# Optimization experiments

Hardware: AMD Instinct MI355X
Metric: run time of the kernel (lower is better)

Reference implementation:

```python
import jax, jax.numpy as jnp
import numpy as np

N, E = 50000, 400000
FN, FE = 128, 128          # in/out node and edge feature dims
W = 256                     # fnns_width
EPS = 1e-5


def _layer_norm(x, g, b):
    m = x.mean(-1, keepdims=True)
    var = x.var(-1, keepdims=True)
    return (x - m) / jnp.sqrt(var + EPS) * g + b


def _fnn(x, params):
    # FNN applies ReLU after EVERY linear, including the last one.
    for w, b in params:
        x = jax.nn.relu(x @ w + b)
    return x


def setup_inputs() -> dict:
    key = jax.random.key(0)
    ks = jax.random.split(key, 32)
    s = 0.05
    d = {
        'v': jax.random.normal(ks[0], (N, FN), jnp.float32),
        'e': jax.random.normal(ks[1], (E, FE), jnp.float32),
        'edge_index': jax.random.randint(ks[2], (2, E), 0, N, jnp.int32),
        # edge branch: LayerNorm over concat width FE + 2*FN = 384
        'edge_ln_g': jnp.ones((FE + 2 * FN,), jnp.float32),
        'edge_ln_b': jnp.zeros((FE + 2 * FN,), jnp.float32),
        'ew0': jax.random.normal(ks[3], (FE + 2 * FN, W), jnp.float32) * s,
        'eb0': jnp.zeros((W,), jnp.float32),
        'ew1': jax.random.normal(ks[4], (W, W), jnp.float32) * s,
        'eb1': jnp.zeros((W,), jnp.float32),
        'ew2': jax.random.normal(ks[5], (W, FE), jnp.float32) * s,
        'eb2': jnp.zeros((FE,), jnp.float32),
        'edge_linear': jax.random.normal(ks[6], (FE, FE), jnp.float32) * s,
        # node branch: LayerNorm over concat width FE + FN = 256
        'node_ln_g': jnp.ones((FE + FN,), jnp.float32),
        'node_ln_b': jnp.zeros((FE + FN,), jnp.float32),
        'nw0': jax.random.normal(ks[7], (FE + FN, W), jnp.float32) * s,
        'nb0': jnp.zeros((W,), jnp.float32),
        'nw1': jax.random.normal(ks[8], (W, W), jnp.float32) * s,
        'nb1': jnp.zeros((W,), jnp.float32),
        'nw2': jax.random.normal(ks[9], (W, FN), jnp.float32) * s,
        'nb2': jnp.zeros((FN,), jnp.float32),
        'node_linear': jax.random.normal(ks[10], (FN, FN), jnp.float32) * s,
    }
    return d


def reference(v, e, edge_index, edge_ln_g, edge_ln_b, ew0, eb0, ew1, eb1,
              ew2, eb2, edge_linear, node_ln_g, node_ln_b, nw0, nb0, nw1,
              nb1, nw2, nb2, node_linear):
    row, col = edge_index[0], edge_index[1]
    n = v.shape[0]
    # edge update: residual linear + FNN(LayerNorm(concat))
    edge_in = jnp.concatenate([e, v[row], v[col]], axis=-1)  # [E, 384]
    e_new = e @ edge_linear + _fnn(
        _layer_norm(edge_in, edge_ln_g, edge_ln_b),
        [(ew0, eb0), (ew1, eb1), (ew2, eb2)])
    # mean scatter-aggregate over destination nodes (col)
    counts = jax.ops.segment_sum(jnp.ones((e.shape[0],), e.dtype), col,
                                 num_segments=n)
    e_aggr = jax.ops.segment_sum(e_new, col, num_segments=n)
    e_aggr = e_aggr / jnp.clip(counts, 1.0)[:, None]
    # node update
    node_in = jnp.concatenate([e_aggr, v], axis=-1)  # [N, 256]
    v_new = v @ node_linear + _fnn(
        _layer_norm(node_in, node_ln_g, node_ln_b),
        [(nw0, nb0), (nw1, nb1), (nw2, nb2)])
    return (v_new, e_new)
```

## Files before the change

### kernel.cpp

```cpp
#include <hip/hip_runtime.h>

typedef _Float16 f16_t;
typedef f16_t f16x4 __attribute__((ext_vector_type(4)));
typedef f16_t f16x8 __attribute__((ext_vector_type(8)));
typedef float f32x4 __attribute__((ext_vector_type(4)));

#define MFMA16(a, b, c) __builtin_amdgcn_mfma_f32_16x16x32_f16((a), (b), (c), 0, 0, 0)

__device__ __forceinline__ float bfr(float x) { return (float)(__bf16)x; }

__global__ void pack_weights_kernel(
    const float* __restrict__ ew0, const float* __restrict__ ew1,
    const float* __restrict__ ew2, const float* __restrict__ eL,
    const float* __restrict__ nw0, const float* __restrict__ nw1,
    const float* __restrict__ nw2, const float* __restrict__ nL,
    f16_t* __restrict__ dst)
{
    int tid = blockIdx.x * 256 + threadIdx.x;
    int fid = tid >> 6, lane = tid & 63;
    const float* src; int Ncols, foff, doff;
    if (fid < 192)      { src = ew0; Ncols = 256; foff = 0;   doff = 0;      }
    else if (fid < 320) { src = ew1; Ncols = 256; foff = 192; doff = 98304;  }
    else if (fid < 384) { src = ew2; Ncols = 128; foff = 320; doff = 163840; }
    else if (fid < 416) { src = eL;  Ncols = 128; foff = 384; doff = 196608; }
    else if (fid < 544) { src = nw0; Ncols = 256; foff = 416; doff = 212992; }
    else if (fid < 672) { src = nw1; Ncols = 256; foff = 544; doff = 278528; }
    else if (fid < 736) { src = nw2; Ncols = 128; foff = 672; doff = 344064; }
    else                { src = nL;  Ncols = 128; foff = 736; doff = 376832; }
    int f = fid - foff;
    int NT = Ncols >> 4;
    int kstep = f / NT, ntile = f - kstep * NT;
    int col = ntile * 16 + (lane & 15);
    int kbase = kstep * 32 + ((lane >> 4) << 3);
    f16x8 out;
    #pragma unroll
    for (int j = 0; j < 8; ++j)
        out[j] = (f16_t)bfr(src[(size_t)(kbase + j) * Ncols + col]);
    *reinterpret_cast<f16x8*>(dst + (size_t)doff + ((size_t)f * 64 + lane) * 8) = out;
}

__launch_bounds__(1024, 8)
__global__ void edge_kernel(
    const float* __restrict__ vfeat, const float* __restrict__ efeat,
    const int* __restrict__ eidx,
    const float* __restrict__ lng, const float* __restrict__ lnb,
    const f16_t* __restrict__ pw,
    const float* __restrict__ b0, const float* __restrict__ b1,
    const float* __restrict__ b2,
    float* __restrict__ out_e, float* __restrict__ aggr, float* __restrict__ cnts,
    int Ee)
{
    __shared__ f16_t XF[24576];
    __shared__ f16_t ERF[8192];
    __shared__ int cidx[64];

    const int t    = threadIdx.x;
    const int lane = t & 63;
    const int wv   = t >> 6;
    const int cw   = wv & 7;
    const int rw   = wv >> 3;
    const size_t ebase = (size_t)blockIdx.x * 64;

    const int el = t >> 4;
    const int pp = t & 15;
    const int et0 = el >> 4;
    const size_t eg0 = ebase + el;
    const int r0 = eidx[eg0];
    const int c0 = eidx[(size_t)Ee + eg0];

    float s = 0.f, sq = 0.f;
    {
        const float4* e4 = (const float4*)efeat;
        const float4* v4 = (const float4*)vfeat;
        #pragma unroll
        for (int i = 0; i < 6; ++i) {
            int q = i * 16 + pp;
            float4 r;
            if (q < 32)      r = e4[eg0 * 32 + q];
            else if (q < 64) r = v4[(size_t)r0 * 32 + (q - 32)];
            else             r = v4[(size_t)c0 * 32 + (q - 64)];
            r.x = bfr(r.x); r.y = bfr(r.y); r.z = bfr(r.z); r.w = bfr(r.w);
            f16x4 h;
            h[0] = (f16_t)r.x; h[1] = (f16_t)r.y; h[2] = (f16_t)r.z; h[3] = (f16_t)r.w;
            int lanep = (el & 15) + 16 * ((q & 7) >> 1);
            int idx = ((q >> 3) * 4 + et0) * 512 + lanep * 8 + (q & 1) * 4;
            *reinterpret_cast<f16x4*>(&XF[idx]) = h;
            if (q < 32)
                *reinterpret_cast<f16x4*>(&ERF[idx]) = h;
            s  += r.x + r.y + r.z + r.w;
            sq += r.x*r.x + r.y*r.y + r.z*r.z + r.w*r.w;
        }
        if (pp == 0) {
            cidx[el] = c0;
            unsafeAtomicAdd(&cnts[c0], 1.0f);
        }
    }
    #pragma unroll
    for (int off = 1; off < 16; off <<= 1) {
        s  += __shfl_xor(s, off);
        sq += __shfl_xor(sq, off);
    }
    const float mean = s * (1.f / 384.f);
    const float rstd = 1.f / sqrtf(sq * (1.f / 384.f) - mean * mean + 1e-5f);

    {
        const float4* g4p = (const float4*)lng;
        const float4* bpp = (const float4*)lnb;
        #pragma unroll
        for (int i = 0; i < 6; ++i) {
            int q = i * 16 + pp;
            int lanep = (el & 15) + 16 * ((q & 7) >> 1);
            int idx = ((q >> 3) * 4 + et0) * 512 + lanep * 8 + (q & 1) * 4;
            f16x4 h = *reinterpret_cast<f16x4*>(&XF[idx]);
            float4 g = g4p[q]; float4 bb = bpp[q];
            h[0] = (f16_t)(((float)h[0] - mean) * rstd * bfr(g.x) + bfr(bb.x));
            h[1] = (f16_t)(((float)h[1] - mean) * rstd * bfr(g.y) + bfr(bb.y));
            h[2] = (f16_t)(((float)h[2] - mean) * rstd * bfr(g.z) + bfr(bb.z));
            h[3] = (f16_t)(((float)h[3] - mean) * rstd * bfr(g.w) + bfr(bb.w));
            *reinterpret_cast<f16x4*>(&XF[idx]) = h;
        }
    }
    __syncthreads();

    const int r16 = lane & 15;
    const int g4i = lane >> 4;

    {
        f32x4 acc[2][2] = {};
        const f16_t* bw = pw;
        #pragma unroll
        for (int ks = 0; ks < 12; ++ks) {
            f16x8 wa0 = *reinterpret_cast<const f16x8*>(
                &bw[((size_t)(ks * 16 + cw * 2 + 0) * 64 + lane) * 8]);
            f16x8 wa1 = *reinterpret_cast<const f16x8*>(
                &bw[((size_t)(ks * 16 + cw * 2 + 1) * 64 + lane) * 8]);
            #pragma unroll
            for (int e2 = 0; e2 < 2; ++e2) {
                f16x8 xb = *reinterpret_cast<const f16x8*>(
                    &XF[(ks * 4 + rw * 2 + e2) * 512 + lane * 8]);
                acc[e2][0] = MFMA16(wa0, xb, acc[e2][0]);
                acc[e2][1] = MFMA16(wa1, xb, acc[e2][1]);
            }
        }
        __syncthreads();
        #pragma unroll
        for (int F2 = 0; F2 < 2; ++F2) {
            int cbase = (cw * 2 + F2) * 16 + g4i * 4;
            float4 bs = *reinterpret_cast<const float4*>(&b0[cbase]);
            float bias[4] = { bfr(bs.x), bfr(bs.y), bfr(bs.z), bfr(bs.w) };
            int lane2 = r16 + 16 * ((cbase & 31) >> 3);
            int j0 = cbase & 7;
            #pragma unroll
            for (int e2 = 0; e2 < 2; ++e2) {
                f16x4 hv;
                #pragma unroll
                for (int qi = 0; qi < 4; ++qi)
                    hv[qi] = (f16_t)fmaxf(acc[e2][F2][qi] + bias[qi], 0.f);
                int idx = ((cbase >> 5) * 4 + rw * 2 + e2) * 512 + lane2 * 8 + j0;
                *reinterpret_cast<f16x4*>(&XF[idx]) = hv;
            }
        }
    }
    __syncthreads();

    {
        f32x4 acc[2][2] = {};
        const f16_t* bw = pw + 98304;
        #pragma unroll
        for (int ks = 0; ks < 8; ++ks) {
            f16x8 wa0 = *reinterpret_cast<const f16x8*>(
                &bw[((size_t)(ks * 16 + cw * 2 + 0) * 64 + lane) * 8]);
            f16x8 wa1 = *reinterpret_cast<const f16x8*>(
                &bw[((size_t)(ks * 16 + cw * 2 + 1) * 64 + lane) * 8]);
            #pragma unroll
            for (int e2 = 0; e2 < 2; ++e2) {
                f16x8 xb = *reinterpret_cast<const f16x8*>(
                    &XF[(ks * 4 + rw * 2 + e2) * 512 + lane * 8]);
                acc[e2][0] = MFMA16(wa0, xb, acc[e2][0]);
                acc[e2][1] = MFMA16(wa1, xb, acc[e2][1]);
            }
        }
        __syncthreads();
        #pragma unroll
        for (int F2 = 0; F2 < 2; ++F2) {
            int cbase = (cw * 2 + F2) * 16 + g4i * 4;
            float4 bs = *reinterpret_cast<const float4*>(&b1[cbase]);
            float bias[4] = { bfr(bs.x), bfr(bs.y), bfr(bs.z), bfr(bs.w) };
            int lane2 = r16 + 16 * ((cbase & 31) >> 3);
            int j0 = cbase & 7;
            #pragma unroll
            for (int e2 = 0; e2 < 2; ++e2) {
                f16x4 hv;
                #pragma unroll
                for (int qi = 0; qi < 4; ++qi)
                    hv[qi] = (f16_t)fmaxf(acc[e2][F2][qi] + bias[qi], 0.f);
                int idx = ((cbase >> 5) * 4 + rw * 2 + e2) * 512 + lane2 * 8 + j0;
                *reinterpret_cast<f16x4*>(&XF[idx]) = hv;
            }
        }
    }
    __syncthreads();

    {
        f32x4 accF[2] = {}, accR[2] = {};
        const f16_t* bw = pw + 163840;
        #pragma unroll
        for (int ks = 0; ks < 8; ++ks) {
            f16x8 wb = *reinterpret_cast<const f16x8*>(
                &bw[((size_t)(ks * 8 + cw) * 64 + lane) * 8]);
            #pragma unroll
            for (int e2 = 0; e2 < 2; ++e2) {
                f16x8 xa = *reinterpret_cast<const f16x8*>(
                    &XF[(ks * 4 + rw * 2 + e2) * 512 + lane * 8]);
                accF[e2] = MFMA16(xa, wb, accF[e2]);
            }
        }
        const f16_t* bwL = pw + 196608;
        #pragma unroll
        for (int ks = 0; ks < 4; ++ks) {
            f16x8 wb = *reinterpret_cast<const f16x8*>(
                &bwL[((size_t)(ks * 8 + cw) * 64 + lane) * 8]);
            #pragma unroll
            for (int e2 = 0; e2 < 2; ++e2) {
                f16x8 ea = *reinterpret_cast<const f16x8*>(
                    &ERF[(ks * 4 + rw * 2 + e2) * 512 + lane * 8]);
                accR[e2] = MFMA16(ea, wb, accR[e2]);
            }
        }
        int c = cw * 16 + r16;
        float bias = bfr(b2[c]);
        #pragma unroll
        for (int e2 = 0; e2 < 2; ++e2)
            #pragma unroll
            for (int qi = 0; qi < 4; ++qi) {
                int rr = (rw * 2 + e2) * 16 + g4i * 4 + qi;
                float val = accR[e2][qi] + fmaxf(accF[e2][qi] + bias, 0.f);
                size_t eg2 = ebase + rr;
                out_e[eg2 * 128 + c] = val;
                unsafeAtomicAdd(&aggr[(size_t)cidx[rr] * 128 + c], val);
            }
    }
}

__launch_bounds__(512, 6)
__global__ void node_kernel(
    const float* __restrict__ vfeat, const float* __restrict__ aggr,
    const float* __restrict__ cnts,
    const float* __restrict__ lng, const float* __restrict__ lnb,
    const f16_t* __restrict__ pw,
    const float* __restrict__ b0, const float* __restrict__ b1,
    const float* __restrict__ b2,
    float* __restrict__ out_v, int Nn)
{
    __shared__ f16_t X[32 * 264];
    __shared__ f16_t H1[32 * 264];

    const int t    = threadIdx.x;
    const int lane = t & 63;
    const int wv   = t >> 6;
    const size_t nbase = (size_t)blockIdx.x * 32;

    const int nl = t >> 4;
    const int pp = t & 15;
    const size_t ng = nbase + nl;
    const bool valid = ng < (size_t)Nn;

    float4 d[4];
    float s = 0.f, sq = 0.f;
    {
        float cmax = 1.f;
        if (valid) cmax = fmaxf(cnts[ng], 1.f);
        const float4* a4 = (const float4*)aggr;
        const float4* v4 = (const float4*)vfeat;
        #pragma unroll
        for (int i = 0; i < 4; ++i) {
            int q = i * 16 + pp;
            float4 r = make_float4(0.f, 0.f, 0.f, 0.f);
            if (valid) {
                if (q < 32) {
                    r = a4[ng * 32 + q];
                    r.x = r.x / cmax; r.y = r.y / cmax;
                    r.z = r.z / cmax; r.w = r.w / cmax;
                } else {
                    float4 rv = v4[ng * 32 + (q - 32)];
                    r.x = bfr(rv.x); r.y = bfr(rv.y); r.z = bfr(rv.z); r.w = bfr(rv.w);
                }
            }
            d[i] = r;
            s  += r.x + r.y + r.z + r.w;
            sq += r.x*r.x + r.y*r.y + r.z*r.z + r.w*r.w;
        }
    }
    #pragma unroll
    for (int off = 1; off < 16; off <<= 1) {
        s  += __shfl_xor(s, off);
        sq += __shfl_xor(sq, off);
    }
    const float mean = s * (1.f / 256.f);
    const float rstd = 1.f / sqrtf(sq * (1.f / 256.f) - mean * mean + 1e-5f);
    {
        const float4* g4p = (const float4*)lng;
        const float4* bpp = (const float4*)lnb;
        #pragma unroll
        for (int i = 0; i < 4; ++i) {
            int q = i * 16 + pp;
            float4 g = g4p[q]; float4 bb = bpp[q];
            f16x4 y;
            y[0] = (f16_t)((d[i].x - mean) * rstd * bfr(g.x) + bfr(bb.x));
            y[1] = (f16_t)((d[i].y - mean) * rstd * bfr(g.y) + bfr(bb.y));
            y[2] = (f16_t)((d[i].z - mean) * rstd * bfr(g.z) + bfr(bb.z));
            y[3] = (f16_t)((d[i].w - mean) * rstd * bfr(g.w) + bfr(bb.w));
            *reinterpret_cast<f16x4*>(&X[nl * 264 + q * 4]) = y;
        }
    }
    __syncthreads();

    const int r16 = lane & 15;
    const int g4i = lane >> 4;
    const int cb4 = g4i * 4;

    {
        f32x4 acc[2][2] = {};
        const f16_t* bw = pw;
        #pragma unroll
        for (int ks = 0; ks < 8; ++ks) {
            f16x8 wa0 = *reinterpret_cast<const f16x8*>(
                &bw[((size_t)(ks * 16 + wv * 2 + 0) * 64 + lane) * 8]);
            f16x8 wa1 = *reinterpret_cast<const f16x8*>(
                &bw[((size_t)(ks * 16 + wv * 2 + 1) * 64 + lane) * 8]);
            #pragma unroll
            for (int nt = 0; nt < 2; ++nt) {
                f16x8 xb = *reinterpret_cast<const f16x8*>(
                    &X[(nt * 16 + r16) * 264 + ks * 32 + g4i * 8]);
                acc[nt][0] = MFMA16(wa0, xb, acc[nt][0]);
                acc[nt][1] = MFMA16(wa1, xb, acc[nt][1]);
            }
        }
        #pragma unroll
        for (int j = 0; j < 2; ++j) {
            int cb = (wv * 2 + j) * 16 + cb4;
            float4 bs = *reinterpret_cast<const float4*>(&b0[cb]);
            float bias[4] = { bfr(bs.x), bfr(bs.y), bfr(bs.z), bfr(bs.w) };
            #pragma unroll
            for (int nt = 0; nt < 2; ++nt) {
                f16x4 hv;
                #pragma unroll
                for (int qi = 0; qi < 4; ++qi)
                    hv[qi] = (f16_t)fmaxf(acc[nt][j][qi] + bias[qi], 0.f);
                *reinterpret_cast<f16x4*>(&H1[(nt * 16 + r16) * 264 + cb]) = hv;
            }
        }
    }
    __syncthreads();

    {
        f32x4 acc[2][2] = {};
        const f16_t* bw = pw + 65536;
        #pragma unroll
        for (int ks = 0; ks < 8; ++ks) {
            f16x8 wa0 = *reinterpret_cast<const f16x8*>(
                &bw[((size_t)(ks * 16 + wv * 2 + 0) * 64 + lane) * 8]);
            f16x8 wa1 = *reinterpret_cast<const f16x8*>(
                &bw[((size_t)(ks * 16 + wv * 2 + 1) * 64 + lane) * 8]);
            #pragma unroll
            for (int nt = 0; nt < 2; ++nt) {
                f16x8 xb = *reinterpret_cast<const f16x8*>(
                    &H1[(nt * 16 + r16) * 264 + ks * 32 + g4i * 8]);
                acc[nt][0] = MFMA16(wa0, xb, acc[nt][0]);
                acc[nt][1] = MFMA16(wa1, xb, acc[nt][1]);
            }
        }
        __syncthreads();
        #pragma unroll
        for (int j = 0; j < 2; ++j) {
            int cb = (wv * 2 + j) * 16 + cb4;
            float4 bs = *reinterpret_cast<const float4*>(&b1[cb]);
            float bias[4] = { bfr(bs.x), bfr(bs.y), bfr(bs.z), bfr(bs.w) };
            #pragma unroll
            for (int nt = 0; nt < 2; ++nt) {
                f16x4 hv;
                #pragma unroll
                for (int qi = 0; qi < 4; ++qi)
                    hv[qi] = (f16_t)fmaxf(acc[nt][j][qi] + bias[qi], 0.f);
                *reinterpret_cast<f16x4*>(&X[(nt * 16 + r16) * 264 + cb]) = hv;
            }
        }
    }
    __syncthreads();

    {
        f32x4 accF[2] = {}, accR[2] = {};
        const f16_t* bw = pw + 131072;
        #pragma unroll
        for (int ks = 0; ks < 8; ++ks) {
            f16x8 wb = *reinterpret_cast<const f16x8*>(
                &bw[((size_t)(ks * 8 + wv) * 64 + lane) * 8]);
            #pragma unroll
            for (int nt = 0; nt < 2; ++nt) {
                f16x8 xa = *reinterpret_cast<const f16x8*>(
                    &X[(nt * 16 + r16) * 264 + ks * 32 + g4i * 8]);
                accF[nt] = MFMA16(xa, wb, accF[nt]);
            }
        }
        const f16_t* bwL = pw + 163840;
        #pragma unroll
        for (int ks = 0; ks < 4; ++ks) {
            f16x8 wb = *reinterpret_cast<const f16x8*>(
                &bwL[((size_t)(ks * 8 + wv) * 64 + lane) * 8]);
            #pragma unroll
            for (int nt = 0; nt < 2; ++nt) {
                size_t rv = nbase + (size_t)(nt * 16 + r16);
                if (rv >= (size_t)Nn) rv = (size_t)Nn - 1;
                const float4* src = (const float4*)&vfeat[rv * 128 + ks * 32 + g4i * 8];
                float4 f0 = src[0];
                float4 f1 = src[1];
                f16x8 va;
                va[0] = (f16_t)bfr(f0.x); va[1] = (f16_t)bfr(f0.y);
                va[2] = (f16_t)bfr(f0.z); va[3] = (f16_t)bfr(f0.w);
                va[4] = (f16_t)bfr(f1.x); va[5] = (f16_t)bfr(f1.y);
                va[6] = (f16_t)bfr(f1.z); va[7] = (f16_t)bfr(f1.w);
                accR[nt] = MFMA16(va, wb, accR[nt]);
            }
        }
        int c = wv * 16 + r16;
        float bias = bfr(b2[c]);
        #pragma unroll
        for (int nt = 0; nt < 2; ++nt)
            #pragma unroll
            for (int qi = 0; qi < 4; ++qi) {
                int rr = nt * 16 + cb4 + qi;
                size_t ng2 = nbase + rr;
                if (ng2 < (size_t)Nn) {
                    float val = accR[nt][qi] + fmaxf(accF[nt][qi] + bias, 0.f);
                    out_v[ng2 * 128 + c] = val;
                }
            }
    }
}

extern "C" void kernel_launch(void* const* d_in, const int* in_sizes, int n_in,
                              void* d_out, int out_size, void* d_ws, size_t ws_size,
                              hipStream_t stream)
{
    const float* v    = (const float*)d_in[0];
    const float* e    = (const float*)d_in[1];
    const int*   eidx = (const int*)d_in[2];
    const float* elng = (const float*)d_in[3];
    const float* elnb = (const float*)d_in[4];
    const float* ew0  = (const float*)d_in[5];
    const float* eb0  = (const float*)d_in[6];
    const float* ew1  = (const float*)d_in[7];
    const float* eb1  = (const float*)d_in[8];
    const float* ew2  = (const float*)d_in[9];
    const float* eb2  = (const float*)d_in[10];
    const float* eLin = (const float*)d_in[11];
    const float* nlng = (const float*)d_in[12];
    const float* nlnb = (const float*)d_in[13];
    const float* nw0  = (const float*)d_in[14];
    const float* nb0  = (const float*)d_in[15];
    const float* nw1  = (const float*)d_in[16];
    const float* nb1  = (const float*)d_in[17];
    const float* nw2  = (const float*)d_in[18];
    const float* nb2  = (const float*)d_in[19];
    const float* nLin = (const float*)d_in[20];

    const int Nn = in_sizes[0] / 128;
    const int Ee = in_sizes[1] / 128;

    float* out_v = (float*)d_out;
    float* out_e = out_v + (size_t)Nn * 128;

    float* aggr = (float*)d_ws;
    float* cnts = aggr + (size_t)Nn * 128;
    f16_t* packw = (f16_t*)((char*)d_ws + (size_t)Nn * 129 * 4);

    hipMemsetAsync(d_ws, 0, (size_t)Nn * 129 * 4, stream);

    pack_weights_kernel<<<192, 256, 0, stream>>>(ew0, ew1, ew2, eLin,
                                                 nw0, nw1, nw2, nLin, packw);

    edge_kernel<<<(Ee + 63) / 64, 1024, 0, stream>>>(v, e, eidx, elng, elnb, packw,
                                                     eb0, eb1, eb2, out_e, aggr, cnts, Ee);

    node_kernel<<<(Nn + 31) / 32, 512, 0, stream>>>(v, aggr, cnts, nlng, nlnb,
                                                    packw + 212992, nb0, nb1, nb2,
                                                    out_v, Nn);
}
```

Measured before the change: 483.3 us.

## Remap edge kernel waves: each wave owns one output tile across all edges

```diff
diff --git a/kernel.cpp b/kernel.cpp
--- a/kernel.cpp
+++ b/kernel.cpp
@@ -50,158 +50,157 @@
     float* __restrict__ out_e, float* __restrict__ aggr, float* __restrict__ cnts,
     int Ee)
 {
-    __shared__ f16_t XF[24576];
-    __shared__ f16_t ERF[8192];
+    __shared__ f16_t XF[12 * 4 * 512];
+    __shared__ f16_t ERF[4 * 4 * 512];
+    __shared__ float SB[64 * 8];
     __shared__ int cidx[64];
 
     const int t    = threadIdx.x;
     const int lane = t & 63;
     const int wv   = t >> 6;
-    const int cw   = wv & 7;
-    const int rw   = wv >> 3;
+    const int r16  = lane & 15;
+    const int g4i  = lane >> 4;
     const size_t ebase = (size_t)blockIdx.x * 64;
 
-    const int el = t >> 4;
-    const int pp = t & 15;
-    const int et0 = el >> 4;
-    const size_t eg0 = ebase + el;
+    const int et_  = wv >> 2;
+    const int sq4  = wv & 3;
+    const int edge = et_ * 16 + r16;
+    const int slot = sq4 * 4 + g4i;
+    const size_t eg0 = ebase + edge;
     const int r0 = eidx[eg0];
     const int c0 = eidx[(size_t)Ee + eg0];
 
+    f16x8 oct[3];
     float s = 0.f, sq = 0.f;
     {
         const float4* e4 = (const float4*)efeat;
         const float4* v4 = (const float4*)vfeat;
-        #pragma unroll
-        for (int i = 0; i < 6; ++i) {
-            int q = i * 16 + pp;
-            float4 r;
-            if (q < 32)      r = e4[eg0 * 32 + q];
-            else if (q < 64) r = v4[(size_t)r0 * 32 + (q - 32)];
-            else             r = v4[(size_t)c0 * 32 + (q - 64)];
-            r.x = bfr(r.x); r.y = bfr(r.y); r.z = bfr(r.z); r.w = bfr(r.w);
-            f16x4 h;
-            h[0] = (f16_t)r.x; h[1] = (f16_t)r.y; h[2] = (f16_t)r.z; h[3] = (f16_t)r.w;
-            int lanep = (el & 15) + 16 * ((q & 7) >> 1);
-            int idx = ((q >> 3) * 4 + et0) * 512 + lanep * 8 + (q & 1) * 4;
-            *reinterpret_cast<f16x4*>(&XF[idx]) = h;
-            if (q < 32)
-                *reinterpret_cast<f16x4*>(&ERF[idx]) = h;
-            s  += r.x + r.y + r.z + r.w;
-            sq += r.x*r.x + r.y*r.y + r.z*r.z + r.w*r.w;
-        }
-        if (pp == 0) {
-            cidx[el] = c0;
+        const float4* srcs[3];
+        srcs[0] = &e4[eg0 * 32 + slot * 2];
+        srcs[1] = &v4[(size_t)r0 * 32 + slot * 2];
+        srcs[2] = &v4[(size_t)c0 * 32 + slot * 2];
+        #pragma unroll
+        for (int i = 0; i < 3; ++i) {
+            float4 f0 = srcs[i][0];
+            float4 f1 = srcs[i][1];
+            float x0 = bfr(f0.x), x1 = bfr(f0.y), x2 = bfr(f0.z), x3 = bfr(f0.w);
+            float x4 = bfr(f1.x), x5 = bfr(f1.y), x6 = bfr(f1.z), x7 = bfr(f1.w);
+            s  += x0 + x1 + x2 + x3 + x4 + x5 + x6 + x7;
+            sq += x0*x0 + x1*x1 + x2*x2 + x3*x3 + x4*x4 + x5*x5 + x6*x6 + x7*x7;
+            f16x8 h;
+            h[0] = (f16_t)x0; h[1] = (f16_t)x1; h[2] = (f16_t)x2; h[3] = (f16_t)x3;
+            h[4] = (f16_t)x4; h[5] = (f16_t)x5; h[6] = (f16_t)x6; h[7] = (f16_t)x7;
+            oct[i] = h;
+        }
+        *reinterpret_cast<f16x8*>(&ERF[(sq4 * 4 + et_) * 512 + lane * 8]) = oct[0];
+        if (slot == 0) {
+            cidx[edge] = c0;
             unsafeAtomicAdd(&cnts[c0], 1.0f);
         }
     }
-    #pragma unroll
-    for (int off = 1; off < 16; off <<= 1) {
-        s  += __shfl_xor(s, off);
-        sq += __shfl_xor(sq, off);
-    }
-    const float mean = s * (1.f / 384.f);
-    const float rstd = 1.f / sqrtf(sq * (1.f / 384.f) - mean * mean + 1e-5f);
-
-    {
+    s  += __shfl_xor(s, 16);  s  += __shfl_xor(s, 32);
+    sq += __shfl_xor(sq, 16); sq += __shfl_xor(sq, 32);
+    if (g4i == 0)
+        *reinterpret_cast<float2*>(&SB[edge * 8 + sq4 * 2]) = make_float2(s, sq);
+    __syncthreads();
+
+    {
+        float4 p0 = *reinterpret_cast<const float4*>(&SB[edge * 8]);
+        float4 p1 = *reinterpret_cast<const float4*>(&SB[edge * 8 + 4]);
+        float S = p0.x + p0.z + p1.x + p1.z;
+        float Q = p0.y + p0.w + p1.y + p1.w;
+        const float mean = S * (1.f / 384.f);
+        const float rstd = 1.f / sqrtf(Q * (1.f / 384.f) - mean * mean + 1e-5f);
         const float4* g4p = (const float4*)lng;
         const float4* bpp = (const float4*)lnb;
         #pragma unroll
-        for (int i = 0; i < 6; ++i) {
-            int q = i * 16 + pp;
-            int lanep = (el & 15) + 16 * ((q & 7) >> 1);
-            int idx = ((q >> 3) * 4 + et0) * 512 + lanep * 8 + (q & 1) * 4;
-            f16x4 h = *reinterpret_cast<f16x4*>(&XF[idx]);
-            float4 g = g4p[q]; float4 bb = bpp[q];
-            h[0] = (f16_t)(((float)h[0] - mean) * rstd * bfr(g.x) + bfr(bb.x));
-            h[1] = (f16_t)(((float)h[1] - mean) * rstd * bfr(g.y) + bfr(bb.y));
-            h[2] = (f16_t)(((float)h[2] - mean) * rstd * bfr(g.z) + bfr(bb.z));
-            h[3] = (f16_t)(((float)h[3] - mean) * rstd * bfr(g.w) + bfr(bb.w));
-            *reinterpret_cast<f16x4*>(&XF[idx]) = h;
-        }
-    }
-    __syncthreads();
-
-    const int r16 = lane & 15;
-    const int g4i = lane >> 4;
-
-    {
-        f32x4 acc[2][2] = {};
+        for (int i = 0; i < 3; ++i) {
+            int q = (i * 16 + slot) * 2;
+            float4 g0 = g4p[q], g1 = g4p[q + 1];
+            float4 bb0 = bpp[q], bb1 = bpp[q + 1];
+            f16x8 h = oct[i];
+            f16x8 y;
+            y[0] = (f16_t)(((float)h[0] - mean) * rstd * bfr(g0.x) + bfr(bb0.x));
+            y[1] = (f16_t)(((float)h[1] - mean) * rstd * bfr(g0.y) + bfr(bb0.y));
+            y[2] = (f16_t)(((float)h[2] - mean) * rstd * bfr(g0.z) + bfr(bb0.z));
+            y[3] = (f16_t)(((float)h[3] - mean) * rstd * bfr(g0.w) + bfr(bb0.w));
+            y[4] = (f16_t)(((float)h[4] - mean) * rstd * bfr(g1.x) + bfr(bb1.x));
+            y[5] = (f16_t)(((float)h[5] - mean) * rstd * bfr(g1.y) + bfr(bb1.y));
+            y[6] = (f16_t)(((float)h[6] - mean) * rstd * bfr(g1.z) + bfr(bb1.z));
+            y[7] = (f16_t)(((float)h[7] - mean) * rstd * bfr(g1.w) + bfr(bb1.w));
+            int ks = i * 4 + sq4;
+            *reinterpret_cast<f16x8*>(&XF[(ks * 4 + et_) * 512 + lane * 8]) = y;
+        }
+    }
+    __syncthreads();
+
+    {
+        f32x4 acc[4] = {};
         const f16_t* bw = pw;
         #pragma unroll
         for (int ks = 0; ks < 12; ++ks) {
-            f16x8 wa0 = *reinterpret_cast<const f16x8*>(
-                &bw[((size_t)(ks * 16 + cw * 2 + 0) * 64 + lane) * 8]);
-            f16x8 wa1 = *reinterpret_cast<const f16x8*>(
-                &bw[((size_t)(ks * 16 + cw * 2 + 1) * 64 + lane) * 8]);
-            #pragma unroll
-            for (int e2 = 0; e2 < 2; ++e2) {
+            f16x8 wa = *reinterpret_cast<const f16x8*>(
+                &bw[((size_t)(ks * 16 + wv) * 64 + lane) * 8]);
+            #pragma unroll
+            for (int et = 0; et < 4; ++et) {
                 f16x8 xb = *reinterpret_cast<const f16x8*>(
-                    &XF[(ks * 4 + rw * 2 + e2) * 512 + lane * 8]);
-                acc[e2][0] = MFMA16(wa0, xb, acc[e2][0]);
-                acc[e2][1] = MFMA16(wa1, xb, acc[e2][1]);
+                    &XF[(ks * 4 + et) * 512 + lane * 8]);
+                acc[et] = MFMA16(wa, xb, acc[et]);
             }
         }
         __syncthreads();
-        #pragma unroll
-        for (int F2 = 0; F2 < 2; ++F2) {
-            int cbase = (cw * 2 + F2) * 16 + g4i * 4;
-            float4 bs = *reinterpret_cast<const float4*>(&b0[cbase]);
-            float bias[4] = { bfr(bs.x), bfr(bs.y), bfr(bs.z), bfr(bs.w) };
-            int lane2 = r16 + 16 * ((cbase & 31) >> 3);
-            int j0 = cbase & 7;
-            #pragma unroll
-            for (int e2 = 0; e2 < 2; ++e2) {
-                f16x4 hv;
-                #pragma unroll
-                for (int qi = 0; qi < 4; ++qi)
-                    hv[qi] = (f16_t)fmaxf(acc[e2][F2][qi] + bias[qi], 0.f);
-                int idx = ((cbase >> 5) * 4 + rw * 2 + e2) * 512 + lane2 * 8 + j0;
-                *reinterpret_cast<f16x4*>(&XF[idx]) = hv;
-            }
-        }
-    }
-    __syncthreads();
-
-    {
-        f32x4 acc[2][2] = {};
+        int cb = wv * 16 + g4i * 4;
+        float4 bs = *reinterpret_cast<const float4*>(&b0[cb]);
+        float bias[4] = { bfr(bs.x), bfr(bs.y), bfr(bs.z), bfr(bs.w) };
+        int ks2 = wv >> 1;
+        int lane2 = r16 + 16 * ((wv & 1) * 2 + (g4i >> 1));
+        int j0 = (g4i & 1) * 4;
+        #pragma unroll
+        for (int et = 0; et < 4; ++et) {
+            f16x4 hv;
+            #pragma unroll
+            for (int qi = 0; qi < 4; ++qi)
+                hv[qi] = (f16_t)fmaxf(acc[et][qi] + bias[qi], 0.f);
+            *reinterpret_cast<f16x4*>(&XF[(ks2 * 4 + et) * 512 + lane2 * 8 + j0]) = hv;
+        }
+    }
+    __syncthreads();
+
+    {
+        f32x4 acc[4] = {};
         const f16_t* bw = pw + 98304;
         #pragma unroll
         for (int ks = 0; ks < 8; ++ks) {
-            f16x8 wa0 = *reinterpret_cast<const f16x8*>(
-                &bw[((size_t)(ks * 16 + cw * 2 + 0) * 64 + lane) * 8]);
-            f16x8 wa1 = *reinterpret_cast<const f16x8*>(
-                &bw[((size_t)(ks * 16 + cw * 2 + 1) * 64 + lane) * 8]);
-            #pragma unroll
-            for (int e2 = 0; e2 < 2; ++e2) {
+            f16x8 wa = *reinterpret_cast<const f16x8*>(
+                &bw[((size_t)(ks * 16 + wv) * 64 + lane) * 8]);
+            #pragma unroll
+            for (int et = 0; et < 4; ++et) {
                 f16x8 xb = *reinterpret_cast<const f16x8*>(
-                    &XF[(ks * 4 + rw * 2 + e2) * 512 + lane * 8]);
-                acc[e2][0] = MFMA16(wa0, xb, acc[e2][0]);
-                acc[e2][1] = MFMA16(wa1, xb, acc[e2][1]);
+                    &XF[(ks * 4 + et) * 512 + lane * 8]);
+                acc[et] = MFMA16(wa, xb, acc[et]);
             }
         }
         __syncthreads();
-        #pragma unroll
-        for (int F2 = 0; F2 < 2; ++F2) {
-            int cbase = (cw * 2 + F2) * 16 + g4i * 4;
-            float4 bs = *reinterpret_cast<const float4*>(&b1[cbase]);
-            float bias[4] = { bfr(bs.x), bfr(bs.y), bfr(bs.z), bfr(bs.w) };
-            int lane2 = r16 + 16 * ((cbase & 31) >> 3);
-            int j0 = cbase & 7;
-            #pragma unroll
-            for (int e2 = 0; e2 < 2; ++e2) {
-                f16x4 hv;
-                #pragma unroll
-                for (int qi = 0; qi < 4; ++qi)
-                    hv[qi] = (f16_t)fmaxf(acc[e2][F2][qi] + bias[qi], 0.f);
-                int idx = ((cbase >> 5) * 4 + rw * 2 + e2) * 512 + lane2 * 8 + j0;
-                *reinterpret_cast<f16x4*>(&XF[idx]) = hv;
-            }
-        }
-    }
-    __syncthreads();
-
-    {
+        int cb = wv * 16 + g4i * 4;
+        float4 bs = *reinterpret_cast<const float4*>(&b1[cb]);
+        float bias[4] = { bfr(bs.x), bfr(bs.y), bfr(bs.z), bfr(bs.w) };
+        int ks2 = wv >> 1;
+        int lane2 = r16 + 16 * ((wv & 1) * 2 + (g4i >> 1));
+        int j0 = (g4i & 1) * 4;
+        #pragma unroll
+        for (int et = 0; et < 4; ++et) {
+            f16x4 hv;
+            #pragma unroll
+            for (int qi = 0; qi < 4; ++qi)
+                hv[qi] = (f16_t)fmaxf(acc[et][qi] + bias[qi], 0.f);
+            *reinterpret_cast<f16x4*>(&XF[(ks2 * 4 + et) * 512 + lane2 * 8 + j0]) = hv;
+        }
+    }
+    __syncthreads();
+
+    {
+        const int cw = wv & 7;
+        const int rw = wv >> 3;
         f32x4 accF[2] = {}, accR[2] = {};
         const f16_t* bw = pw + 163840;
         #pragma unroll
```

Result: faster. 446.7 us (-7.6%).
